# Kernel tuning notes

Measured on AMD Instinct MI355X. Metric: run time of the kernel, lower is better.

Reference implementation:

```python
import jax, jax.numpy as jnp
import numpy as np

EPS = 1e-8
TAU = 1.0


def graph_conv(h_in, adj, W, b):
    # h: [N, D_out]
    h = h_in @ W
    nrm = jnp.linalg.norm(h, axis=1, keepdims=True)
    h_norm = h / jnp.maximum(nrm, EPS)  # F.normalize with eps clamp
    # cosine-sim logits + log-adjacency mask -> row softmax
    logits = (h_norm @ h_norm.T) / TAU + jnp.log(adj + EPS)  # [N, N]
    attn = jax.nn.softmax(logits, axis=1)
    return attn @ h + b


def setup_inputs() -> dict:
    key = jax.random.key(0)
    ks = jax.random.split(key, 20)
    N, F, H, C = 4096, 512, 128, 16

    def xavier(k, fan_in, fan_out):
        s = float(np.sqrt(6.0 / (fan_in + fan_out)))
        return jax.random.uniform(k, (fan_in, fan_out), minval=-s, maxval=s, dtype=jnp.float32)

    return {
        "x": jax.random.normal(ks[0], (N, F), dtype=jnp.float32),
        "adj_low": jax.random.uniform(ks[1], (N, N), dtype=jnp.float32),
        "adj_high": jax.random.uniform(ks[2], (N, N), dtype=jnp.float32),
        "adj_mid": jax.random.uniform(ks[3], (N, N), dtype=jnp.float32),
        "w_low0": xavier(ks[4], F, H), "b_low0": jnp.zeros((H,), jnp.float32),
        "w_high0": xavier(ks[5], F, H), "b_high0": jnp.zeros((H,), jnp.float32),
        "w_mid0": xavier(ks[6], F, H), "b_mid0": jnp.zeros((H,), jnp.float32),
        "w_low1": xavier(ks[7], H, C), "b_low1": jnp.zeros((C,), jnp.float32),
        "w_high1": xavier(ks[8], H, C), "b_high1": jnp.zeros((C,), jnp.float32),
        "w_mid1": xavier(ks[9], H, C), "b_mid1": jnp.zeros((C,), jnp.float32),
        "g0": jnp.ones((3,), jnp.float32),
        "g1": jnp.ones((3,), jnp.float32),
    }


def reference(x, adj_low, adj_high, adj_mid,
              w_low0, b_low0, w_high0, b_high0, w_mid0, b_mid0,
              w_low1, b_low1, w_high1, b_high1, w_mid1, b_mid1,
              g0, g1):
    # layer 0 (inner layer: ReLU; dropout p=0 in eval mode -> identity)
    hl = jax.nn.relu(graph_conv(x, adj_low, w_low0, b_low0))
    hh = jax.nn.relu(graph_conv(x, adj_high, w_high0, b_high0))
    hm = jax.nn.relu(graph_conv(x, adj_mid, w_mid0, b_mid0))
    w = jax.nn.softmax(g0)
    h = w[0] * hl + w[1] * hh + w[2] * hm

    # layer 1 (final layer: no activation)
    hl = graph_conv(h, adj_low, w_low1, b_low1)
    hh = graph_conv(h, adj_high, w_high1, b_high1)
    hm = graph_conv(h, adj_mid, w_mid1, b_mid1)
    w = jax.nn.softmax(g1)
    h = w[0] * hl + w[1] * hh + w[2] * hm

    return jax.nn.log_softmax(h, axis=-1)
```

## Files before the change

### kernel.cpp

```cpp
#include <hip/hip_runtime.h>

#define N_NODES 4096
#define F_IN 512
#define H_DIM 128
#define C_DIM 16
#define EPSF 1e-8f
#define LOG2E 1.4426950408889634f
#define SMAX 2.0f
#define NKS0 8
#define KLEN0 (N_NODES / NKS0)
#define NT0 (KLEN0 / 32)
#define NKS1 8

typedef __attribute__((ext_vector_type(8))) short bf16x8;
typedef __attribute__((ext_vector_type(4))) short bf16x4;
typedef __attribute__((ext_vector_type(4))) float f32x4;

__device__ __forceinline__ ushort f2bf(float f){
  union { float f; unsigned u; } v; v.f = f;
  unsigned u = v.u;
  return (ushort)((u + 0x7fffu + ((u >> 16) & 1u)) >> 16);
}
__device__ __forceinline__ float bf2f(ushort h){
  union { unsigned u; float f; } v; v.u = ((unsigned)h) << 16;
  return v.f;
}

__global__ __launch_bounds__(256) void proj0_kernel(
    const float* __restrict__ x,
    const float* __restrict__ Wl, const float* __restrict__ Wh,
    const float* __restrict__ Wm,
    ushort* __restrict__ hn, ushort* __restrict__ hvT)
{
  const int t = threadIdx.x;
  const int d = t & 127;
  const int half = t >> 7;
  const int r0 = blockIdx.x * 8;
  __shared__ float xs[8][F_IN];
  for (int i = t; i < 8 * F_IN; i += 256)
    xs[i >> 9][i & 511] = x[(size_t)(r0 + (i >> 9)) * F_IN + (i & 511)];
  __syncthreads();

  float acc0[8], acc1[8], acc2[8];
#pragma unroll
  for (int r = 0; r < 8; r++) { acc0[r] = 0.f; acc1[r] = 0.f; acc2[r] = 0.f; }

  const int k0 = half * (F_IN / 2);
  for (int k = k0; k < k0 + F_IN / 2; k++) {
    float wl = Wl[k * H_DIM + d];
    float wh = Wh[k * H_DIM + d];
    float wm = Wm[k * H_DIM + d];
#pragma unroll
    for (int r = 0; r < 8; r++) {
      float xv = xs[r][k];
      acc0[r] = fmaf(xv, wl, acc0[r]);
      acc1[r] = fmaf(xv, wh, acc1[r]);
      acc2[r] = fmaf(xv, wm, acc2[r]);
    }
  }

  __shared__ float part[3][8][128];
  if (half == 1) {
#pragma unroll
    for (int r = 0; r < 8; r++) {
      part[0][r][d] = acc0[r]; part[1][r][d] = acc1[r]; part[2][r][d] = acc2[r];
    }
  }
  __syncthreads();
  if (half == 0) {
#pragma unroll
    for (int r = 0; r < 8; r++) {
      acc0[r] += part[0][r][d]; acc1[r] += part[1][r][d]; acc2[r] += part[2][r][d];
    }
  }

  __shared__ float red[24][2];
  const int wv = t >> 6;
  const int lane = t & 63;

#define REDUCE_BRANCH(ACC, B)                                        \
  _Pragma("unroll")                                                  \
  for (int r = 0; r < 8; r++) {                                      \
    float v = ACC[r] * ACC[r];                                       \
    v += __shfl_down(v, 32); v += __shfl_down(v, 16);                \
    v += __shfl_down(v, 8);  v += __shfl_down(v, 4);                 \
    v += __shfl_down(v, 2);  v += __shfl_down(v, 1);                 \
    if (lane == 0) red[(B) * 8 + r][wv] = v;                         \
  }
  if (half == 0) {
    REDUCE_BRANCH(acc0, 0)
    REDUCE_BRANCH(acc1, 1)
    REDUCE_BRANCH(acc2, 2)
  }
  __syncthreads();

#define WRITE_BRANCH(ACC, B)                                                   \
  _Pragma("unroll")                                                            \
  for (int r = 0; r < 8; r++) {                                                \
    float nrm = sqrtf(red[(B) * 8 + r][0] + red[(B) * 8 + r][1]);              \
    float rn = 1.0f / fmaxf(nrm, EPSF);                                        \
    float h = ACC[r];                                                          \
    hn[((size_t)(B) * N_NODES + r0 + r) * H_DIM + d] = f2bf(h * rn);           \
    hvT[((size_t)(B) * H_DIM + d) * N_NODES + r0 + r] = f2bf(h);               \
  }
  if (half == 0) {
    WRITE_BRANCH(acc0, 0)
    WRITE_BRANCH(acc1, 1)
    WRITE_BRANCH(acc2, 2)
  }
#undef REDUCE_BRANCH
#undef WRITE_BRANCH
}

__global__ __launch_bounds__(256) void flash0_kernel(
    const ushort* __restrict__ hn, const ushort* __restrict__ hvT,
    const float* __restrict__ adj_l, const float* __restrict__ adj_h,
    const float* __restrict__ adj_m,
    float* __restrict__ pl0, ushort* __restrict__ pO)
{
  const int tid = threadIdx.x;
  const int w = tid >> 6;
  const int lane = tid & 63;
  const int lr = lane & 15;
  const int lg = lane >> 4;
  const int ks = blockIdx.y;
  const int b = blockIdx.z;
  const int q0 = blockIdx.x * 64 + w * 16;
  const float* adj = (b == 0) ? adj_l : (b == 1) ? adj_h : adj_m;
  const ushort* Qg = hn + (size_t)b * N_NODES * H_DIM;
  const ushort* VTg = hvT + (size_t)b * H_DIM * N_NODES;
  const int kbase = ks * KLEN0;

  __shared__ ushort sK[2][32 * 128];
  __shared__ ushort sV[2][128 * 32];

  bf16x8 qf[4];
  {
    const ushort* qp = Qg + (size_t)(q0 + lr) * H_DIM + lg * 8;
#pragma unroll
    for (int u = 0; u < 4; u++) qf[u] = *(const bf16x8*)(qp + 32 * u);
  }

  f32x4 o[8];
#pragma unroll
  for (int dt = 0; dt < 8; dt++) o[dt] = (f32x4){0.f, 0.f, 0.f, 0.f};
  float lsum = 0.f;

  const float* arow = adj + (size_t)(q0 + lr) * N_NODES + kbase;

  const int sA = w * 128 + lane;
  const int sB = sA + 64;
  const int kkA = sA >> 4, kcA = sA & 15;
  const int kkB = sB >> 4, kcB = sB & 15;
  const size_t kOffA = (size_t)kkA * H_DIM + ((size_t)(kcA ^ (kkA & 7)) << 3);
  const size_t kOffB = (size_t)kkB * H_DIM + ((size_t)(kcB ^ (kkB & 7)) << 3);
  const int dA = sA >> 2, vcA = sA & 3;
  const int dB = sB >> 2, vcB = sB & 3;
  const size_t vOffA = (size_t)dA * N_NODES + ((size_t)(vcA ^ ((dA >> 1) & 3)) << 3);
  const size_t vOffB = (size_t)dB * N_NODES + ((size_t)(vcB ^ ((dB >> 1) & 3)) << 3);

#define STAGE(BUF, K0)                                                         \
  {                                                                            \
    const ushort* ksrc = Qg + (size_t)(K0) * H_DIM;                            \
    const ushort* vsrc = VTg + (K0);                                           \
    __builtin_amdgcn_global_load_lds(ksrc + kOffA,                             \
        (char*)&sK[BUF][0] + w * 2048, 16, 0, 0);                              \
    __builtin_amdgcn_global_load_lds(ksrc + kOffB,                             \
        (char*)&sK[BUF][0] + w * 2048 + 1024, 16, 0, 0);                       \
    __builtin_amdgcn_global_load_lds(vsrc + vOffA,                             \
        (char*)&sV[BUF][0] + w * 2048, 16, 0, 0);                              \
    __builtin_amdgcn_global_load_lds(vsrc + vOffB,                             \
        (char*)&sV[BUF][0] + w * 2048 + 1024, 16, 0, 0);                       \
  }

  STAGE(0, kbase)

  for (int t = 0; t < NT0; t++) {
    const int cur = t & 1;
    __syncthreads();
    if (t + 1 < NT0) STAGE(cur ^ 1, kbase + (t + 1) * 32)

    f32x4 a0 = *(const f32x4*)(arow + t * 32 + lg * 4);
    f32x4 a1 = *(const f32x4*)(arow + t * 32 + 16 + lg * 4);

    f32x4 s0 = (f32x4){0.f, 0.f, 0.f, 0.f};
    f32x4 s1 = (f32x4){0.f, 0.f, 0.f, 0.f};
    const char* sKc = (const char*)&sK[cur][0];
#pragma unroll
    for (int u = 0; u < 4; u++) {
      const int c0 = lg + 4 * u;
      bf16x8 kf0 = *(const bf16x8*)(sKc + lr * 256 + ((c0 ^ (lr & 7)) << 4));
      bf16x8 kf1 = *(const bf16x8*)(sKc + (lr + 16) * 256 + ((c0 ^ (lr & 7)) << 4));
      s0 = __builtin_amdgcn_mfma_f32_16x16x32_bf16(kf0, qf[u], s0, 0, 0, 0);
      s1 = __builtin_amdgcn_mfma_f32_16x16x32_bf16(kf1, qf[u], s1, 0, 0, 0);
    }
    bf16x4 pf0, pf1;
#pragma unroll
    for (int r = 0; r < 4; r++) {
      float p0 = exp2f(fmaf(s0[r], LOG2E, -SMAX)) * (a0[r] + EPSF);
      float p1 = exp2f(fmaf(s1[r], LOG2E, -SMAX)) * (a1[r] + EPSF);
      lsum += p0 + p1;
      pf0[r] = (short)f2bf(p0);
      pf1[r] = (short)f2bf(p1);
    }
    const char* sVc = (const char*)&sV[cur][0];
#pragma unroll
    for (int dt = 0; dt < 8; dt++) {
      const int dd = dt * 16 + lr;
      const int sw = (dd >> 1) & 3;
      bf16x4 vf0 = *(const bf16x4*)(sVc + dd * 64 +
                     ((((lg >> 1) + 0) ^ sw) << 4) + (lg & 1) * 8);
      bf16x4 vf1 = *(const bf16x4*)(sVc + dd * 64 +
                     ((((lg >> 1) + 2) ^ sw) << 4) + (lg & 1) * 8);
      o[dt] = __builtin_amdgcn_mfma_f32_16x16x16bf16_1k(pf0, vf0, o[dt], 0, 0, 0);
      o[dt] = __builtin_amdgcn_mfma_f32_16x16x16bf16_1k(pf1, vf1, o[dt], 0, 0, 0);
    }
  }
#undef STAGE

  const int ps = b * NKS0 + ks;
  float psum = lsum;
  psum += __shfl_xor(psum, 16);
  psum += __shfl_xor(psum, 32);
  if (lg == 0) pl0[(size_t)ps * N_NODES + q0 + lr] = psum;
#pragma unroll
  for (int dt = 0; dt < 8; dt++) {
#pragma unroll
    for (int r = 0; r < 4; r++) {
      pO[((size_t)ps * N_NODES + q0 + lg * 4 + r) * H_DIM + dt * 16 + lr] =
          f2bf(o[dt][r]);
    }
  }
}

__global__ __launch_bounds__(128) void mix1_kernel(
    const float* __restrict__ pl0, const ushort* __restrict__ pO,
    const float* __restrict__ bl0, const float* __restrict__ bh0,
    const float* __restrict__ bm0,
    const float* __restrict__ Wl1, const float* __restrict__ Wh1,
    const float* __restrict__ Wm1,
    const float* __restrict__ g0,
    ushort* __restrict__ hn1b, ushort* __restrict__ hbT)
{
  const int q = blockIdx.x;
  const int t = threadIdx.x;
  float ga = g0[0], gb = g0[1], gc = g0[2];
  float gm = fmaxf(ga, fmaxf(gb, gc));
  float e0 = expf(ga - gm), e1 = expf(gb - gm), e2 = expf(gc - gm);
  float ei = 1.0f / (e0 + e1 + e2);

  __shared__ float Ls[3];
  if (t < 3) {
    float L = 0.f;
#pragma unroll
    for (int ks = 0; ks < NKS0; ks++) L += pl0[(size_t)(t * NKS0 + ks) * N_NODES + q];
    Ls[t] = L;
  }
  float O0 = 0.f, O1 = 0.f, O2 = 0.f;
#pragma unroll
  for (int ks = 0; ks < NKS0; ks++) {
    O0 += bf2f(pO[((size_t)(0 * NKS0 + ks) * N_NODES + q) * H_DIM + t]);
    O1 += bf2f(pO[((size_t)(1 * NKS0 + ks) * N_NODES + q) * H_DIM + t]);
    O2 += bf2f(pO[((size_t)(2 * NKS0 + ks) * N_NODES + q) * H_DIM + t]);
  }
  __syncthreads();

  __shared__ float hc[H_DIM];
  hc[t] = e0 * ei * fmaxf(O0 / Ls[0] + bl0[t], 0.f)
        + e1 * ei * fmaxf(O1 / Ls[1] + bh0[t], 0.f)
        + e2 * ei * fmaxf(O2 / Ls[2] + bm0[t], 0.f);
  __syncthreads();

  __shared__ float shb[48];
  if (t < 48) {
    const int b = t >> 4, j = t & 15;
    const float* W = (b == 0) ? Wl1 : (b == 1) ? Wh1 : Wm1;
    float s = 0.f;
    for (int k = 0; k < H_DIM; k++) s = fmaf(hc[k], W[k * C_DIM + j], s);
    shb[t] = s;
  }
  __syncthreads();
  __shared__ float rns[3];
  if (t < 3) {
    float s = 0.f;
#pragma unroll
    for (int j = 0; j < C_DIM; j++) { float u = shb[t * C_DIM + j]; s = fmaf(u, u, s); }
    rns[t] = 1.0f / fmaxf(sqrtf(s), EPSF);
  }
  __syncthreads();
  if (t < 48) {
    const int b = t >> 4, j = t & 15;
    hbT[((size_t)b * C_DIM + j) * N_NODES + q] = f2bf(shb[t]);
    hn1b[((size_t)b * N_NODES + q) * C_DIM + j] = f2bf(shb[t] * rns[b]);
  }
}

__global__ __launch_bounds__(256) void flash1_kernel(
    const ushort* __restrict__ hn1b, const ushort* __restrict__ hbT,
    const float* __restrict__ adj_l, const float* __restrict__ adj_h,
    const float* __restrict__ adj_m,
    float* __restrict__ pl, float* __restrict__ pacc)
{
  const int tid = threadIdx.x;
  const int wid = tid >> 6;
  const int lane = tid & 63;
  const int lr = lane & 15;
  const int lg = lane >> 4;
  const int qblk = blockIdx.x * 64;
  const int q0 = qblk + wid * 16;
  const int ks = blockIdx.y;
  const int b = blockIdx.z;
  const float* adj = (b == 0) ? adj_l : (b == 1) ? adj_h : adj_m;
  const ushort* Qn = hn1b + (size_t)b * N_NODES * C_DIM;
  const ushort* VT = hbT + (size_t)b * C_DIM * N_NODES;
  const int kbase = ks * (N_NODES / NKS1);
  const int nt = (N_NODES / NKS1) / 32;

  __shared__ float sAdj[2][64 * 32];

  const bf16x4 qf = *(const bf16x4*)(Qn + (size_t)(q0 + lr) * C_DIM + lg * 4);
  const f32x4 zero = (f32x4){0.f, 0.f, 0.f, 0.f};
  f32x4 o = zero;
  float lsum = 0.f;
  const ushort* vrow = VT + (size_t)lr * N_NODES;

  const int rowA = tid >> 3, cA = tid & 7;
  const int rowB = rowA + 32;
  const size_t aOffA = (size_t)rowA * N_NODES + ((size_t)(cA ^ (rowA & 7)) << 2);
  const size_t aOffB = (size_t)rowB * N_NODES + ((size_t)(cA ^ (rowB & 7)) << 2);
  const float* adjq = adj + (size_t)qblk * N_NODES;

#define STAGE1(BUF, K0)                                                        \
  {                                                                            \
    const float* asrc = adjq + (K0);                                           \
    __builtin_amdgcn_global_load_lds(asrc + aOffA,                             \
        (char*)&sAdj[BUF][0] + wid * 1024, 16, 0, 0);                          \
    __builtin_amdgcn_global_load_lds(asrc + aOffB,                             \
        (char*)&sAdj[BUF][0] + 4096 + wid * 1024, 16, 0, 0);                   \
  }

  STAGE1(0, kbase)

  const int rowL = wid * 16 + lr;
  const int adr0 = rowL * 32 + ((lg ^ (rowL & 7)) << 2);
  const int adr1 = rowL * 32 + (((4 + lg) ^ (rowL & 7)) << 2);

  for (int t = 0; t < nt; t++) {
    const int cur = t & 1;
    __syncthreads();
    if (t + 1 < nt) STAGE1(cur ^ 1, kbase + (t + 1) * 32)

    const int k0 = kbase + t * 32;
    bf16x4 kf0 = *(const bf16x4*)(Qn + (size_t)(k0 + lr) * C_DIM + lg * 4);
    bf16x4 kf1 = *(const bf16x4*)(Qn + (size_t)(k0 + 16 + lr) * C_DIM + lg * 4);
    f32x4 s0 = __builtin_amdgcn_mfma_f32_16x16x16bf16_1k(kf0, qf, zero, 0, 0, 0);
    f32x4 s1 = __builtin_amdgcn_mfma_f32_16x16x16bf16_1k(kf1, qf, zero, 0, 0, 0);
    f32x4 a0 = *(const f32x4*)&sAdj[cur][adr0];
    f32x4 a1 = *(const f32x4*)&sAdj[cur][adr1];
    bf16x4 pf0, pf1;
#pragma unroll
    for (int r = 0; r < 4; r++) {
      float e0 = exp2f(fmaf(s0[r], LOG2E, -SMAX));
      float e1 = exp2f(fmaf(s1[r], LOG2E, -SMAX));
      float p0 = e0 * (a0[r] + EPSF);
      float p1 = e1 * (a1[r] + EPSF);
      lsum += p0 + p1;
      pf0[r] = (short)f2bf(p0);
      pf1[r] = (short)f2bf(p1);
    }
    bf16x4 vf0 = *(const bf16x4*)(vrow + k0 + lg * 4);
    bf16x4 vf1 = *(const bf16x4*)(vrow + k0 + 16 + lg * 4);
    o = __builtin_amdgcn_mfma_f32_16x16x16bf16_1k(pf0, vf0, o, 0, 0, 0);
    o = __builtin_amdgcn_mfma_f32_16x16x16bf16_1k(pf1, vf1, o, 0, 0, 0);
  }
#undef STAGE1

  const int ps = b * NKS1 + ks;
  float psum = lsum;
  psum += __shfl_xor(psum, 16);
  psum += __shfl_xor(psum, 32);
  if (lg == 0) pl[(size_t)ps * N_NODES + q0 + lr] = psum;
#pragma unroll
  for (int r = 0; r < 4; r++)
    pacc[((size_t)ps * N_NODES + q0 + lg * 4 + r) * C_DIM + lr] = o[r];
}

__global__ __launch_bounds__(256) void combine1_kernel(
    const float* __restrict__ pl, const float* __restrict__ pacc,
    float* __restrict__ o1)
{
  const int q = blockIdx.x * 256 + threadIdx.x;
  const int b = blockIdx.y;
  float L = 0.f;
  f32x4 out0 = (f32x4){0,0,0,0}, out1 = (f32x4){0,0,0,0},
        out2 = (f32x4){0,0,0,0}, out3 = (f32x4){0,0,0,0};
#pragma unroll
  for (int ks = 0; ks < NKS1; ks++) {
    const size_t pidx = (size_t)(b * NKS1 + ks) * N_NODES + q;
    L += pl[pidx];
    const f32x4* pa = (const f32x4*)(pacc + pidx * C_DIM);
    out0 += pa[0]; out1 += pa[1]; out2 += pa[2]; out3 += pa[3];
  }
  float invL = 1.0f / L;
  f32x4* dst = (f32x4*)(o1 + ((size_t)b * N_NODES + q) * C_DIM);
  dst[0] = out0 * invL; dst[1] = out1 * invL; dst[2] = out2 * invL; dst[3] = out3 * invL;
}

__global__ __launch_bounds__(256) void final_kernel(
    const float* __restrict__ o1,
    const float* __restrict__ bl1, const float* __restrict__ bh1,
    const float* __restrict__ bm1,
    const float* __restrict__ g1, float* __restrict__ out)
{
  const int q = blockIdx.x * 256 + threadIdx.x;
  float ga = g1[0], gb = g1[1], gc = g1[2];
  float gm = fmaxf(ga, fmaxf(gb, gc));
  float e0 = expf(ga - gm), e1 = expf(gb - gm), e2 = expf(gc - gm);
  float ei = 1.0f / (e0 + e1 + e2);
  float w0 = e0 * ei, w1 = e1 * ei, w2 = e2 * ei;
  const size_t NC = (size_t)N_NODES * C_DIM;

  float v[16];
#pragma unroll
  for (int i = 0; i < 4; i++) {
    f32x4 a = ((const f32x4*)(o1 + (size_t)q * C_DIM))[i];
    f32x4 bA = ((const f32x4*)(o1 + NC + (size_t)q * C_DIM))[i];
    f32x4 c = ((const f32x4*)(o1 + 2 * NC + (size_t)q * C_DIM))[i];
    f32x4 xl = ((const f32x4*)bl1)[i];
    f32x4 xh = ((const f32x4*)bh1)[i];
    f32x4 xm = ((const f32x4*)bm1)[i];
#pragma unroll
    for (int j = 0; j < 4; j++)
      v[i * 4 + j] = w0 * (a[j] + xl[j]) + w1 * (bA[j] + xh[j]) + w2 * (c[j] + xm[j]);
  }
  float mx = -1e30f;
#pragma unroll
  for (int j = 0; j < 16; j++) mx = fmaxf(mx, v[j]);
  float se = 0.f;
#pragma unroll
  for (int j = 0; j < 16; j++) se += expf(v[j] - mx);
  float lse = mx + logf(se);
  f32x4* dst = (f32x4*)(out + (size_t)q * C_DIM);
#pragma unroll
  for (int i = 0; i < 4; i++) {
    f32x4 r;
#pragma unroll
    for (int j = 0; j < 4; j++) r[j] = v[i * 4 + j] - lse;
    dst[i] = r;
  }
}

extern "C" void kernel_launch(void* const* d_in, const int* in_sizes, int n_in,
                              void* d_out, int out_size, void* d_ws, size_t ws_size,
                              hipStream_t stream) {
  (void)in_sizes; (void)n_in; (void)out_size; (void)ws_size;
  const float* x     = (const float*)d_in[0];
  const float* adj_l = (const float*)d_in[1];
  const float* adj_h = (const float*)d_in[2];
  const float* adj_m = (const float*)d_in[3];
  const float* w_l0  = (const float*)d_in[4];
  const float* b_l0  = (const float*)d_in[5];
  const float* w_h0  = (const float*)d_in[6];
  const float* b_h0  = (const float*)d_in[7];
  const float* w_m0  = (const float*)d_in[8];
  const float* b_m0  = (const float*)d_in[9];
  const float* w_l1  = (const float*)d_in[10];
  const float* b_l1  = (const float*)d_in[11];
  const float* w_h1  = (const float*)d_in[12];
  const float* b_h1  = (const float*)d_in[13];
  const float* w_m1  = (const float*)d_in[14];
  const float* b_m1  = (const float*)d_in[15];
  const float* g0    = (const float*)d_in[16];
  const float* g1    = (const float*)d_in[17];
  float* out = (float*)d_out;

  char* ws = (char*)d_ws;
  ushort* hn  = (ushort*)(ws);
  ushort* hvT = (ushort*)(ws + (3u << 20));
  ushort* hn1b= (ushort*)(ws + (6u << 20));
  ushort* hbT = (ushort*)(ws + (6u << 20) + (384u << 10));
  float*  pl0 = (float*)(ws + (12u << 20));
  ushort* pO  = (ushort*)(ws + (12u << 20) + (512u << 10));
  float*  pl  = (float*)(ws + (12u << 20));
  float*  pacc= (float*)(ws + (13u << 20));
  float*  o1  = (float*)(ws + (20u << 20));

  proj0_kernel<<<dim3(512), dim3(256), 0, stream>>>(x, w_l0, w_h0, w_m0, hn, hvT);
  flash0_kernel<<<dim3(64, NKS0, 3), dim3(256), 0, stream>>>(hn, hvT, adj_l, adj_h, adj_m,
                                                             pl0, pO);
  mix1_kernel<<<dim3(4096), dim3(128), 0, stream>>>(pl0, pO, b_l0, b_h0, b_m0,
                                                    w_l1, w_h1, w_m1, g0, hn1b, hbT);
  flash1_kernel<<<dim3(64, NKS1, 3), dim3(256), 0, stream>>>(hn1b, hbT, adj_l, adj_h, adj_m,
                                                             pl, pacc);
  combine1_kernel<<<dim3(16, 3), dim3(256), 0, stream>>>(pl, pacc, o1);
  final_kernel<<<dim3(16), dim3(256), 0, stream>>>(o1, b_l1, b_h1, b_m1, g1, out);
}
```

Before: 168.3 us.

## Triple-buffer K/V LDS staging and prefetch adjacency two tiles ahead

Result: no change. 165.3 us (-1.8%).

```diff
diff --git a/kernel.cpp b/kernel.cpp
--- a/kernel.cpp
+++ b/kernel.cpp
@@ -131,8 +131,8 @@
   const ushort* VTg = hvT + (size_t)b * H_DIM * N_NODES;
   const int kbase = ks * KLEN0;
 
-  __shared__ ushort sK[2][32 * 128];
-  __shared__ ushort sV[2][128 * 32];
+  __shared__ ushort sK[3][32 * 128];
+  __shared__ ushort sV[3][128 * 32];
 
   bf16x8 qf[4];
   {
@@ -173,19 +173,36 @@
         (char*)&sV[BUF][0] + w * 2048 + 1024, 16, 0, 0);                       \
   }
 
+  f32x4 a0c, a1c, a0n, a1n, a0n2, a1n2;
   STAGE(0, kbase)
-
+  a0c = *(const f32x4*)(arow + lg * 4);
+  a1c = *(const f32x4*)(arow + 16 + lg * 4);
+  STAGE(1, kbase + 32)
+  a0n = *(const f32x4*)(arow + 32 + lg * 4);
+  a1n = *(const f32x4*)(arow + 48 + lg * 4);
+
+  int bufc = 0;
   for (int t = 0; t < NT0; t++) {
-    const int cur = t & 1;
-    __syncthreads();
-    if (t + 1 < NT0) STAGE(cur ^ 1, kbase + (t + 1) * 32)
-
-    f32x4 a0 = *(const f32x4*)(arow + t * 32 + lg * 4);
-    f32x4 a1 = *(const f32x4*)(arow + t * 32 + 16 + lg * 4);
+    __builtin_amdgcn_sched_barrier(0);
+    __builtin_amdgcn_s_barrier();
+    __builtin_amdgcn_sched_barrier(0);
+    if (t + 2 < NT0) {
+      const int b2 = (bufc + 2 > 2) ? (bufc + 2 - 3) : (bufc + 2);
+      STAGE(b2, kbase + (t + 2) * 32)
+      a0n2 = *(const f32x4*)(arow + (t + 2) * 32 + lg * 4);
+      a1n2 = *(const f32x4*)(arow + (t + 2) * 32 + 16 + lg * 4);
+    }
+    const int rem = NT0 - 1 - t;
+    if (rem >= 2)      { asm volatile("s_waitcnt vmcnt(12)" ::: "memory"); }
+    else if (rem == 1) { asm volatile("s_waitcnt vmcnt(6)"  ::: "memory"); }
+    else               { asm volatile("s_waitcnt vmcnt(0)"  ::: "memory"); }
+    __builtin_amdgcn_sched_barrier(0);
+    __builtin_amdgcn_s_barrier();
+    __builtin_amdgcn_sched_barrier(0);
 
     f32x4 s0 = (f32x4){0.f, 0.f, 0.f, 0.f};
     f32x4 s1 = (f32x4){0.f, 0.f, 0.f, 0.f};
-    const char* sKc = (const char*)&sK[cur][0];
+    const char* sKc = (const char*)&sK[bufc][0];
 #pragma unroll
     for (int u = 0; u < 4; u++) {
       const int c0 = lg + 4 * u;
@@ -197,13 +214,13 @@
     bf16x4 pf0, pf1;
 #pragma unroll
     for (int r = 0; r < 4; r++) {
-      float p0 = exp2f(fmaf(s0[r], LOG2E, -SMAX)) * (a0[r] + EPSF);
-      float p1 = exp2f(fmaf(s1[r], LOG2E, -SMAX)) * (a1[r] + EPSF);
+      float p0 = exp2f(fmaf(s0[r], LOG2E, -SMAX)) * (a0c[r] + EPSF);
+      float p1 = exp2f(fmaf(s1[r], LOG2E, -SMAX)) * (a1c[r] + EPSF);
       lsum += p0 + p1;
       pf0[r] = (short)f2bf(p0);
       pf1[r] = (short)f2bf(p1);
     }
-    const char* sVc = (const char*)&sV[cur][0];
+    const char* sVc = (const char*)&sV[bufc][0];
 #pragma unroll
     for (int dt = 0; dt < 8; dt++) {
       const int dd = dt * 16 + lr;
@@ -215,6 +232,9 @@
       o[dt] = __builtin_amdgcn_mfma_f32_16x16x16bf16_1k(pf0, vf0, o[dt], 0, 0, 0);
       o[dt] = __builtin_amdgcn_mfma_f32_16x16x16bf16_1k(pf1, vf1, o[dt], 0, 0, 0);
     }
+    a0c = a0n; a1c = a1n;
+    a0n = a0n2; a1n = a1n2;
+    bufc = (bufc == 2) ? 0 : (bufc + 1);
   }
 #undef STAGE
 
```

## Double block size in flash0 and prefetch adjacency with manual waitcnt pipelining

Applied to the files above, without the earlier changes.

After: 164.0 us. -2.6%, faster.

```diff
diff --git a/kernel.cpp b/kernel.cpp
--- a/kernel.cpp
+++ b/kernel.cpp
@@ -112,7 +112,7 @@
 #undef WRITE_BRANCH
 }
 
-__global__ __launch_bounds__(256) void flash0_kernel(
+__global__ __launch_bounds__(512) void flash0_kernel(
     const ushort* __restrict__ hn, const ushort* __restrict__ hvT,
     const float* __restrict__ adj_l, const float* __restrict__ adj_h,
     const float* __restrict__ adj_m,
@@ -125,7 +125,7 @@
   const int lg = lane >> 4;
   const int ks = blockIdx.y;
   const int b = blockIdx.z;
-  const int q0 = blockIdx.x * 64 + w * 16;
+  const int q0 = blockIdx.x * 128 + w * 16;
   const float* adj = (b == 0) ? adj_l : (b == 1) ? adj_h : adj_m;
   const ushort* Qg = hn + (size_t)b * N_NODES * H_DIM;
   const ushort* VTg = hvT + (size_t)b * H_DIM * N_NODES;
@@ -148,41 +148,40 @@
 
   const float* arow = adj + (size_t)(q0 + lr) * N_NODES + kbase;
 
-  const int sA = w * 128 + lane;
-  const int sB = sA + 64;
-  const int kkA = sA >> 4, kcA = sA & 15;
-  const int kkB = sB >> 4, kcB = sB & 15;
-  const size_t kOffA = (size_t)kkA * H_DIM + ((size_t)(kcA ^ (kkA & 7)) << 3);
-  const size_t kOffB = (size_t)kkB * H_DIM + ((size_t)(kcB ^ (kkB & 7)) << 3);
-  const int dA = sA >> 2, vcA = sA & 3;
-  const int dB = sB >> 2, vcB = sB & 3;
-  const size_t vOffA = (size_t)dA * N_NODES + ((size_t)(vcA ^ ((dA >> 1) & 3)) << 3);
-  const size_t vOffB = (size_t)dB * N_NODES + ((size_t)(vcB ^ ((dB >> 1) & 3)) << 3);
+  const int kk = tid >> 4, kc = tid & 15;
+  const size_t kOff = (size_t)kk * H_DIM + ((size_t)(kc ^ (kk & 7)) << 3);
+  const int dV = tid >> 2, vc = tid & 3;
+  const size_t vOff = (size_t)dV * N_NODES + ((size_t)(vc ^ ((dV >> 1) & 3)) << 3);
 
 #define STAGE(BUF, K0)                                                         \
   {                                                                            \
-    const ushort* ksrc = Qg + (size_t)(K0) * H_DIM;                            \
-    const ushort* vsrc = VTg + (K0);                                           \
-    __builtin_amdgcn_global_load_lds(ksrc + kOffA,                             \
-        (char*)&sK[BUF][0] + w * 2048, 16, 0, 0);                              \
-    __builtin_amdgcn_global_load_lds(ksrc + kOffB,                             \
-        (char*)&sK[BUF][0] + w * 2048 + 1024, 16, 0, 0);                       \
-    __builtin_amdgcn_global_load_lds(vsrc + vOffA,                             \
-        (char*)&sV[BUF][0] + w * 2048, 16, 0, 0);                              \
-    __builtin_amdgcn_global_load_lds(vsrc + vOffB,                             \
-        (char*)&sV[BUF][0] + w * 2048 + 1024, 16, 0, 0);                       \
-  }
-
+    __builtin_amdgcn_global_load_lds(Qg + (size_t)(K0) * H_DIM + kOff,         \
+        (char*)&sK[BUF][0] + w * 1024, 16, 0, 0);                              \
+    __builtin_amdgcn_global_load_lds(VTg + (K0) + vOff,                        \
+        (char*)&sV[BUF][0] + w * 1024, 16, 0, 0);                              \
+  }
+
+  f32x4 a0c, a1c, a0n, a1n;
   STAGE(0, kbase)
+  a0c = *(const f32x4*)(arow + lg * 4);
+  a1c = *(const f32x4*)(arow + 16 + lg * 4);
 
   for (int t = 0; t < NT0; t++) {
     const int cur = t & 1;
-    __syncthreads();
-    if (t + 1 < NT0) STAGE(cur ^ 1, kbase + (t + 1) * 32)
-
-    f32x4 a0 = *(const f32x4*)(arow + t * 32 + lg * 4);
-    f32x4 a1 = *(const f32x4*)(arow + t * 32 + 16 + lg * 4);
-
+    __builtin_amdgcn_s_barrier();
+    __builtin_amdgcn_sched_barrier(0);
+    if (t + 1 < NT0) {
+      STAGE(cur ^ 1, kbase + (t + 1) * 32)
+      a0n = *(const f32x4*)(arow + (t + 1) * 32 + lg * 4);
+      a1n = *(const f32x4*)(arow + (t + 1) * 32 + 16 + lg * 4);
+    }
+    if (t + 1 < NT0) { asm volatile("s_waitcnt vmcnt(4)" ::: "memory"); }
+    else             { asm volatile("s_waitcnt vmcnt(0)" ::: "memory"); }
+    __builtin_amdgcn_sched_barrier(0);
+    __builtin_amdgcn_s_barrier();
+    __builtin_amdgcn_sched_barrier(0);
+
+    __builtin_amdgcn_s_setprio(1);
     f32x4 s0 = (f32x4){0.f, 0.f, 0.f, 0.f};
     f32x4 s1 = (f32x4){0.f, 0.f, 0.f, 0.f};
     const char* sKc = (const char*)&sK[cur][0];
@@ -197,8 +196,8 @@
     bf16x4 pf0, pf1;
 #pragma unroll
     for (int r = 0; r < 4; r++) {
-      float p0 = exp2f(fmaf(s0[r], LOG2E, -SMAX)) * (a0[r] + EPSF);
-      float p1 = exp2f(fmaf(s1[r], LOG2E, -SMAX)) * (a1[r] + EPSF);
+      float p0 = exp2f(fmaf(s0[r], LOG2E, -SMAX)) * (a0c[r] + EPSF);
+      float p1 = exp2f(fmaf(s1[r], LOG2E, -SMAX)) * (a1c[r] + EPSF);
       lsum += p0 + p1;
       pf0[r] = (short)f2bf(p0);
       pf1[r] = (short)f2bf(p1);
@@ -215,6 +214,8 @@
       o[dt] = __builtin_amdgcn_mfma_f32_16x16x16bf16_1k(pf0, vf0, o[dt], 0, 0, 0);
       o[dt] = __builtin_amdgcn_mfma_f32_16x16x16bf16_1k(pf1, vf1, o[dt], 0, 0, 0);
     }
+    __builtin_amdgcn_s_setprio(0);
+    a0c = a0n; a1c = a1n;
   }
 #undef STAGE
 
@@ -486,7 +487,7 @@
   float*  o1  = (float*)(ws + (20u << 20));
 
   proj0_kernel<<<dim3(512), dim3(256), 0, stream>>>(x, w_l0, w_h0, w_m0, hn, hvT);
-  flash0_kernel<<<dim3(64, NKS0, 3), dim3(256), 0, stream>>>(hn, hvT, adj_l, adj_h, adj_m,
+  flash0_kernel<<<dim3(32, NKS0, 3), dim3(512), 0, stream>>>(hn, hvT, adj_l, adj_h, adj_m,
                                                              pl0, pO);
   mix1_kernel<<<dim3(4096), dim3(128), 0, stream>>>(pl0, pO, b_l0, b_h0, b_m0,
                                                     w_l1, w_h1, w_m1, g0, hn1b, hbT);
```

## Stage adjacency tiles into LDS via async loads with explicit waitcnt pipelining

Applied to the files above, without the earlier changes.

Result: faster. 162.2 us, median of 2 (-3.6%).

```diff
diff --git a/kernel.cpp b/kernel.cpp
--- a/kernel.cpp
+++ b/kernel.cpp
@@ -125,7 +125,8 @@
   const int lg = lane >> 4;
   const int ks = blockIdx.y;
   const int b = blockIdx.z;
-  const int q0 = blockIdx.x * 64 + w * 16;
+  const int qblk = blockIdx.x * 64;
+  const int q0 = qblk + w * 16;
   const float* adj = (b == 0) ? adj_l : (b == 1) ? adj_h : adj_m;
   const ushort* Qg = hn + (size_t)b * N_NODES * H_DIM;
   const ushort* VTg = hvT + (size_t)b * H_DIM * N_NODES;
@@ -133,6 +134,7 @@
 
   __shared__ ushort sK[2][32 * 128];
   __shared__ ushort sV[2][128 * 32];
+  __shared__ float  sAdj[2][64 * 32];
 
   bf16x8 qf[4];
   {
@@ -145,8 +147,6 @@
 #pragma unroll
   for (int dt = 0; dt < 8; dt++) o[dt] = (f32x4){0.f, 0.f, 0.f, 0.f};
   float lsum = 0.f;
-
-  const float* arow = adj + (size_t)(q0 + lr) * N_NODES + kbase;
 
   const int sA = w * 128 + lane;
   const int sB = sA + 64;
@@ -158,11 +158,17 @@
   const int dB = sB >> 2, vcB = sB & 3;
   const size_t vOffA = (size_t)dA * N_NODES + ((size_t)(vcA ^ ((dA >> 1) & 3)) << 3);
   const size_t vOffB = (size_t)dB * N_NODES + ((size_t)(vcB ^ ((dB >> 1) & 3)) << 3);
+  const int arw1 = tid >> 3, ac1 = tid & 7;
+  const int arw2 = arw1 + 32;
+  const size_t aOff1 = (size_t)arw1 * N_NODES + ((size_t)(ac1 ^ (arw1 & 7)) << 2);
+  const size_t aOff2 = (size_t)arw2 * N_NODES + ((size_t)(ac1 ^ (arw2 & 7)) << 2);
+  const float* adjq = adj + (size_t)qblk * N_NODES;
 
 #define STAGE(BUF, K0)                                                         \
   {                                                                            \
     const ushort* ksrc = Qg + (size_t)(K0) * H_DIM;                            \
     const ushort* vsrc = VTg + (K0);                                           \
+    const float*  asrc = adjq + (K0);                                          \
     __builtin_amdgcn_global_load_lds(ksrc + kOffA,                             \
         (char*)&sK[BUF][0] + w * 2048, 16, 0, 0);                              \
     __builtin_amdgcn_global_load_lds(ksrc + kOffB,                             \
@@ -171,18 +177,30 @@
         (char*)&sV[BUF][0] + w * 2048, 16, 0, 0);                              \
     __builtin_amdgcn_global_load_lds(vsrc + vOffB,                             \
         (char*)&sV[BUF][0] + w * 2048 + 1024, 16, 0, 0);                       \
+    __builtin_amdgcn_global_load_lds(asrc + aOff1,                             \
+        (char*)&sAdj[BUF][0] + w * 1024, 16, 0, 0);                            \
+    __builtin_amdgcn_global_load_lds(asrc + aOff2,                             \
+        (char*)&sAdj[BUF][0] + 4096 + w * 1024, 16, 0, 0);                     \
   }
 
   STAGE(0, kbase)
+
+  const int rL = w * 16 + lr;
+  const int adr0 = rL * 32 + ((lg ^ (rL & 7)) << 2);
+  const int adr1 = rL * 32 + (((4 + lg) ^ (rL & 7)) << 2);
 
   for (int t = 0; t < NT0; t++) {
     const int cur = t & 1;
-    __syncthreads();
+    __builtin_amdgcn_s_barrier();
+    __builtin_amdgcn_sched_barrier(0);
     if (t + 1 < NT0) STAGE(cur ^ 1, kbase + (t + 1) * 32)
-
-    f32x4 a0 = *(const f32x4*)(arow + t * 32 + lg * 4);
-    f32x4 a1 = *(const f32x4*)(arow + t * 32 + 16 + lg * 4);
-
+    if (t + 1 < NT0) { asm volatile("s_waitcnt vmcnt(6)" ::: "memory"); }
+    else             { asm volatile("s_waitcnt vmcnt(0)" ::: "memory"); }
+    __builtin_amdgcn_sched_barrier(0);
+    __builtin_amdgcn_s_barrier();
+    __builtin_amdgcn_sched_barrier(0);
+
+    __builtin_amdgcn_s_setprio(1);
     f32x4 s0 = (f32x4){0.f, 0.f, 0.f, 0.f};
     f32x4 s1 = (f32x4){0.f, 0.f, 0.f, 0.f};
     const char* sKc = (const char*)&sK[cur][0];
@@ -194,6 +212,8 @@
       s0 = __builtin_amdgcn_mfma_f32_16x16x32_bf16(kf0, qf[u], s0, 0, 0, 0);
       s1 = __builtin_amdgcn_mfma_f32_16x16x32_bf16(kf1, qf[u], s1, 0, 0, 0);
     }
+    f32x4 a0 = *(const f32x4*)&sAdj[cur][adr0];
+    f32x4 a1 = *(const f32x4*)&sAdj[cur][adr1];
     bf16x4 pf0, pf1;
 #pragma unroll
     for (int r = 0; r < 4; r++) {
@@ -215,6 +235,7 @@
       o[dt] = __builtin_amdgcn_mfma_f32_16x16x16bf16_1k(pf0, vf0, o[dt], 0, 0, 0);
       o[dt] = __builtin_amdgcn_mfma_f32_16x16x16bf16_1k(pf1, vf1, o[dt], 0, 0, 0);
     }
+    __builtin_amdgcn_s_setprio(0);
   }
 #undef STAGE
 
```
